# Performance work log

Measured on AMD Instinct MI355X. Metric: run time of the kernel, lower is better.

Reference implementation:

```python
import jax, jax.numpy as jnp
import numpy as np

H, DH = 8, 64            # heads, dim_head (module defaults)
B, N, DN, DE = 1, 512, 128, 64  # batch, nodes, node feat, edge feat
INNER = H * DH


def _w(key, fan_in, fan_out):
    return jax.random.normal(key, (fan_in, fan_out), jnp.float32) / np.sqrt(fan_in)


def setup_inputs() -> dict:
    key = jax.random.key(0)
    ks = jax.random.split(key, 8)
    return {
        "nodes": jax.random.normal(ks[0], (B, N, DN), jnp.float32),
        "edges": jax.random.normal(ks[1], (B, N, N, DE), jnp.float32),
        "mask": jnp.ones((B, N), dtype=bool),
        "Wq": _w(ks[2], DN, INNER), "bq": jnp.zeros((INNER,), jnp.float32),
        "Wk": _w(ks[3], DN, INNER), "bk": jnp.zeros((INNER,), jnp.float32),
        "Wv": _w(ks[4], DN, INNER), "bv": jnp.zeros((INNER,), jnp.float32),
        "We": _w(ks[5], DE, INNER), "be": jnp.zeros((INNER,), jnp.float32),
        "Wo": _w(ks[6], INNER, DN), "bo": jnp.zeros((DN,), jnp.float32),
    }


def _split_heads(x):
    # (b, ..., h*d) -> (b*h, ..., d), matching rearrange 'b ... (h d) -> (b h) ... d'
    b = x.shape[0]
    mid = x.shape[1:-1]
    x = x.reshape(b, *mid, H, DH)
    x = jnp.moveaxis(x, -2, 1)              # (b, h, ..., d)
    return x.reshape(b * H, *mid, DH)


def reference(nodes, edges, mask, Wq, bq, Wk, bk, Wv, bv, We, be, Wo, bo):
    scale = DH ** (-0.5)
    q = _split_heads(nodes @ Wq + bq)        # (bh, n, d)
    k = _split_heads(nodes @ Wk + bk)        # (bh, n, d)
    v = _split_heads(nodes @ Wv + bv)        # (bh, n, d)
    e = _split_heads(edges @ We + be)        # (bh, n, n, d) -- ek == ev == e_kv
    k = k[:, None, :, :] + e                 # (bh, i, j, d) per-ij keys
    v = v[:, None, :, :] + e                 # (bh, i, j, d) per-ij values
    sim = jnp.einsum('bid,bijd->bij', q, k) * scale
    m = mask[:, :, None] & mask[:, None, :]  # (b, i, j)
    m = jnp.repeat(m, H, axis=0)             # (bh, i, j)
    sim = jnp.where(m, sim, -jnp.finfo(sim.dtype).max)
    attn = jax.nn.softmax(sim, axis=-1)
    out = jnp.einsum('bij,bijd->bid', attn, v)           # (bh, n, d)
    out = out.reshape(B, H, N, DH).transpose(0, 2, 1, 3).reshape(B, N, INNER)
    return out @ Wo + bo                                  # (b, n, d_node)
```

## Files before the change

kernel.cpp:

```cpp
#include <hip/hip_runtime.h>
#include <hip/hip_bf16.h>

#define NN 512
#define DNODE 128
#define DEDGE 64
#define NH 8
#define DHD 64
#define DIN 512
#define SCALE 0.125f

typedef unsigned short u16;
typedef unsigned int u32;
typedef short bf16x8 __attribute__((ext_vector_type(8)));
typedef float f32x4 __attribute__((ext_vector_type(4)));

__device__ __forceinline__ float bf2f(u16 b) {
    u32 u = ((u32)b) << 16;
    return __builtin_bit_cast(float, u);
}
__device__ __forceinline__ u16 f2bf(float f) {
    u32 u = __builtin_bit_cast(u32, f);
    return (u16)((u + 0x7fffu + ((u >> 16) & 1u)) >> 16);
}
__device__ __forceinline__ float bflo(u32 u) { return __builtin_bit_cast(float, u << 16); }
__device__ __forceinline__ float bfhi(u32 u) { return __builtin_bit_cast(float, u & 0xffff0000u); }

__global__ __launch_bounds__(256) void k_qkv(
    const float* __restrict__ nodes,
    const float* __restrict__ Wq, const float* __restrict__ bq,
    const float* __restrict__ Wk, const float* __restrict__ bk,
    const float* __restrict__ Wv, const float* __restrict__ bv,
    float* __restrict__ Qo, float* __restrict__ Ko, float* __restrict__ Vo)
{
    const int it = blockIdx.x, ct = blockIdx.y, which = blockIdx.z;
    const float* W    = which == 0 ? Wq : (which == 1 ? Wk : Wv);
    const float* bias = which == 0 ? bq : (which == 1 ? bk : bv);
    float* O          = which == 0 ? Qo : (which == 1 ? Ko : Vo);
    __shared__ float As[64][132];
    __shared__ float Bs[128][68];
    const int t = threadIdx.x;
    const int ibase = it * 64, cbase = ct * 64;
#pragma unroll
    for (int p = 0; p < 8; ++p) {
        int r = p * 8 + (t >> 5), c4 = (t & 31) * 4;
        *(float4*)&As[r][c4] = *(const float4*)(nodes + (ibase + r) * DNODE + c4);
    }
#pragma unroll
    for (int p = 0; p < 8; ++p) {
        int k = p * 16 + (t >> 4), c4 = (t & 15) * 4;
        *(float4*)&Bs[k][c4] = *(const float4*)(W + k * DIN + cbase + c4);
    }
    __syncthreads();
    const int tx = t & 15, ty = t >> 4;
    float acc[4][4] = {};
    for (int k = 0; k < DNODE; ++k) {
        float4 b4 = *(const float4*)&Bs[k][tx * 4];
#pragma unroll
        for (int e = 0; e < 4; ++e) {
            float a = As[ty * 4 + e][k];
            acc[e][0] += a * b4.x; acc[e][1] += a * b4.y;
            acc[e][2] += a * b4.z; acc[e][3] += a * b4.w;
        }
    }
    const int h = ct;
#pragma unroll
    for (int ii = 0; ii < 4; ++ii) {
        int i = ibase + ty * 4 + ii;
        float4 o;
        o.x = acc[ii][0] + bias[cbase + tx * 4 + 0];
        o.y = acc[ii][1] + bias[cbase + tx * 4 + 1];
        o.z = acc[ii][2] + bias[cbase + tx * 4 + 2];
        o.w = acc[ii][3] + bias[cbase + tx * 4 + 3];
        *(float4*)(O + ((size_t)h * NN + i) * DHD + tx * 4) = o;
    }
}

__global__ __launch_bounds__(256) void k_qe(
    const float* __restrict__ Q, const float* __restrict__ We, float* __restrict__ QE)
{
    const int it = blockIdx.x, h = blockIdx.y;
    __shared__ float Qs[64][68];
    __shared__ float WsT[64][68];
    const int t = threadIdx.x;
    const int ibase = it * 64;
#pragma unroll
    for (int p = 0; p < 4; ++p) {
        int r = p * 16 + (t >> 4), d4 = (t & 15) * 4;
        *(float4*)&Qs[r][d4] = *(const float4*)(Q + ((size_t)h * NN + ibase + r) * DHD + d4);
    }
#pragma unroll
    for (int p = 0; p < 4; ++p) {
        int c = p * 16 + (t >> 4), d4 = (t & 15) * 4;
        float4 v = *(const float4*)(We + c * DIN + h * DHD + d4);
        WsT[d4 + 0][c] = v.x; WsT[d4 + 1][c] = v.y;
        WsT[d4 + 2][c] = v.z; WsT[d4 + 3][c] = v.w;
    }
    __syncthreads();
    const int tx = t & 15, ty = t >> 4;
    float acc[4][4] = {};
    for (int d = 0; d < DHD; ++d) {
        float4 b4 = *(const float4*)&WsT[d][tx * 4];
#pragma unroll
        for (int e = 0; e < 4; ++e) {
            float a = Qs[ty * 4 + e][d];
            acc[e][0] += a * b4.x; acc[e][1] += a * b4.y;
            acc[e][2] += a * b4.z; acc[e][3] += a * b4.w;
        }
    }
#pragma unroll
    for (int ii = 0; ii < 4; ++ii) {
        int i = ibase + ty * 4 + ii;
        float4 o;
        o.x = SCALE * acc[ii][0]; o.y = SCALE * acc[ii][1];
        o.z = SCALE * acc[ii][2]; o.w = SCALE * acc[ii][3];
        *(float4*)(QE + ((size_t)h * NN + i) * DEDGE + tx * 4) = o;
    }
}

__global__ __launch_bounds__(256) void k_qk(
    const float* __restrict__ Q, const float* __restrict__ K, float* __restrict__ QK)
{
    const int jt = blockIdx.x, it = blockIdx.y, h = blockIdx.z;
    __shared__ float Qs[64][68];
    __shared__ float KsT[64][68];
    const int t = threadIdx.x;
    const int ibase = it * 64, jbase = jt * 64;
#pragma unroll
    for (int p = 0; p < 4; ++p) {
        int r = p * 16 + (t >> 4), d4 = (t & 15) * 4;
        *(float4*)&Qs[r][d4] = *(const float4*)(Q + ((size_t)h * NN + ibase + r) * DHD + d4);
    }
#pragma unroll
    for (int p = 0; p < 4; ++p) {
        int j = p * 16 + (t >> 4), d4 = (t & 15) * 4;
        float4 v = *(const float4*)(K + ((size_t)h * NN + jbase + j) * DHD + d4);
        KsT[d4 + 0][j] = v.x; KsT[d4 + 1][j] = v.y;
        KsT[d4 + 2][j] = v.z; KsT[d4 + 3][j] = v.w;
    }
    __syncthreads();
    const int tx = t & 15, ty = t >> 4;
    float acc[4][4] = {};
    for (int d = 0; d < DHD; ++d) {
        float4 b4 = *(const float4*)&KsT[d][tx * 4];
#pragma unroll
        for (int e = 0; e < 4; ++e) {
            float a = Qs[ty * 4 + e][d];
            acc[e][0] += a * b4.x; acc[e][1] += a * b4.y;
            acc[e][2] += a * b4.z; acc[e][3] += a * b4.w;
        }
    }
#pragma unroll
    for (int ii = 0; ii < 4; ++ii) {
        int i = ibase + ty * 4 + ii;
        float4 o;
        o.x = SCALE * acc[ii][0]; o.y = SCALE * acc[ii][1];
        o.z = SCALE * acc[ii][2]; o.w = SCALE * acc[ii][3];
        *(float4*)(QK + ((size_t)h * NN + i) * NN + jbase + tx * 4) = o;
    }
}

__global__ __launch_bounds__(512, 4) void k_fused(
    const float* __restrict__ edges, const float* __restrict__ QK,
    const float* __restrict__ QE, float* __restrict__ AE, u16* __restrict__ P)
{
    __shared__ u16 erow[NN * 64];
    __shared__ u16 PlT[NH * 520];
    __shared__ float ae_acc[NH * 65];
    __shared__ float wred0[16][9];
    __shared__ float wred1[16][9];
    const int i = blockIdx.x;
    const int t = threadIdx.x;
    const int lane = t & 63, w = t >> 6;
    const int jl = lane & 15, hq = lane >> 4;
    const int h0 = hq * 4;
    const int jw = w * 64;

    const float* E = edges + (size_t)i * NN * DEDGE;
    const int jst = t >> 3, c0 = (t & 7) * 8;
    float4 fa[8], fb[8];
#pragma unroll
    for (int p = 0; p < 8; ++p) {
        const float* s = E + (p * 64 + jst) * 64 + c0;
        fa[p] = *(const float4*)s;
        fb[p] = *(const float4*)(s + 4);
    }
    float qkv[16];
#pragma unroll
    for (int jt = 0; jt < 4; ++jt)
#pragma unroll
        for (int r = 0; r < 4; ++r)
            qkv[jt * 4 + r] = (hq < 2)
                ? QK[((size_t)(h0 + r) * NN + i) * NN + jw + jt * 16 + jl] : 0.f;
    float4 qa0 = {0,0,0,0}, qa1 = qa0, qa2 = qa0, qa3 = qa0;
    if (jl < 8) {
        const float* qe = QE + ((size_t)jl * NN + i) * DEDGE + hq * 8;
        qa0 = *(const float4*)(qe + 0);
        qa1 = *(const float4*)(qe + 4);
        qa2 = *(const float4*)(qe + 32);
        qa3 = *(const float4*)(qe + 36);
    }
    for (int z = t; z < NH * 65; z += 512) ae_acc[z] = 0.f;

    bf16x8 af0, af1;
    af0[0]=(short)f2bf(qa0.x); af0[1]=(short)f2bf(qa0.y); af0[2]=(short)f2bf(qa0.z); af0[3]=(short)f2bf(qa0.w);
    af0[4]=(short)f2bf(qa1.x); af0[5]=(short)f2bf(qa1.y); af0[6]=(short)f2bf(qa1.z); af0[7]=(short)f2bf(qa1.w);
    af1[0]=(short)f2bf(qa2.x); af1[1]=(short)f2bf(qa2.y); af1[2]=(short)f2bf(qa2.z); af1[3]=(short)f2bf(qa2.w);
    af1[4]=(short)f2bf(qa3.x); af1[5]=(short)f2bf(qa3.y); af1[6]=(short)f2bf(qa3.z); af1[7]=(short)f2bf(qa3.w);

#pragma unroll
    for (int p = 0; p < 8; ++p) {
        int j = p * 64 + jst;
        uint4 pk;
        pk.x = (u32)f2bf(fa[p].x) | ((u32)f2bf(fa[p].y) << 16);
        pk.y = (u32)f2bf(fa[p].z) | ((u32)f2bf(fa[p].w) << 16);
        pk.z = (u32)f2bf(fb[p].x) | ((u32)f2bf(fb[p].y) << 16);
        pk.w = (u32)f2bf(fb[p].z) | ((u32)f2bf(fb[p].w) << 16);
        int sb = (j * 128 + c0 * 2) ^ ((j & 7) << 4);
        *(uint4*)((char*)erow + sb) = pk;
    }
    __syncthreads();

    f32x4 acc[4] = {f32x4{0,0,0,0}, f32x4{0,0,0,0}, f32x4{0,0,0,0}, f32x4{0,0,0,0}};
    const char* eb = (const char*)erow;
#pragma unroll
    for (int jt = 0; jt < 4; ++jt) {
        int j = jw + jt * 16 + jl;
        int x = (j & 7) << 4;
        uint4 e0 = *(const uint4*)(eb + ((j * 128 + hq * 16) ^ x));
        uint4 e1 = *(const uint4*)(eb + ((j * 128 + 64 + hq * 16) ^ x));
        f32x4 a = acc[jt];
        a = __builtin_amdgcn_mfma_f32_16x16x32_bf16(af0, __builtin_bit_cast(bf16x8, e0), a, 0, 0, 0);
        a = __builtin_amdgcn_mfma_f32_16x16x32_bf16(af1, __builtin_bit_cast(bf16x8, e1), a, 0, 0, 0);
        acc[jt] = a;
    }
#pragma unroll
    for (int jt = 0; jt < 4; ++jt)
#pragma unroll
        for (int r = 0; r < 4; ++r) acc[jt][r] += qkv[jt * 4 + r];

    float lred[4];
#pragma unroll
    for (int r = 0; r < 4; ++r) {
        float m0 = fmaxf(fmaxf(acc[0][r], acc[1][r]), fmaxf(acc[2][r], acc[3][r]));
        m0 = fmaxf(m0, __shfl_xor(m0, 1));
        m0 = fmaxf(m0, __shfl_xor(m0, 2));
        m0 = fmaxf(m0, __shfl_xor(m0, 4));
        m0 = fmaxf(m0, __shfl_xor(m0, 8));
        lred[r] = m0;
    }
    if (jl == 0 && hq < 2) {
#pragma unroll
        for (int r = 0; r < 4; ++r) wred0[h0 + r][w] = lred[r];
    }
    __syncthreads();
    float mm[4];
#pragma unroll
    for (int r = 0; r < 4; ++r) {
        float m = wred0[h0 + r][0];
#pragma unroll
        for (int ww = 1; ww < 8; ++ww) m = fmaxf(m, wred0[h0 + r][ww]);
        mm[r] = m;
    }
#pragma unroll
    for (int r = 0; r < 4; ++r) {
        float ls = 0.f;
#pragma unroll
        for (int jt = 0; jt < 4; ++jt) {
            float e = __expf(acc[jt][r] - mm[r]);
            acc[jt][r] = e; ls += e;
        }
        ls += __shfl_xor(ls, 1);
        ls += __shfl_xor(ls, 2);
        ls += __shfl_xor(ls, 4);
        ls += __shfl_xor(ls, 8);
        lred[r] = ls;
    }
    if (jl == 0 && hq < 2) {
#pragma unroll
        for (int r = 0; r < 4; ++r) wred1[h0 + r][w] = lred[r];
    }
    __syncthreads();
    if (hq < 2) {
#pragma unroll
        for (int r = 0; r < 4; ++r) {
            float s = wred1[h0 + r][0];
#pragma unroll
            for (int ww = 1; ww < 8; ++ww) s += wred1[h0 + r][ww];
            float inv = 1.f / s;
            int h = h0 + r;
#pragma unroll
            for (int jt = 0; jt < 4; ++jt) {
                int j = jw + jt * 16 + jl;
                u16 pb = f2bf(acc[jt][r] * inv);
                PlT[h * 520 + j] = pb;
                P[((size_t)h * NN + i) * NN + j] = pb;
            }
        }
    }
    __syncthreads();

    const int cp = lane & 31, jh = lane >> 5;
    const int jbase = w * 64 + jh * 32;
    float ae0[8] = {}, ae1[8] = {};
#pragma unroll
    for (int jb = 0; jb < 4; ++jb) {
        int j0 = jbase + jb * 8;
        float elo[8], ehi[8];
#pragma unroll
        for (int k = 0; k < 8; ++k) {
            int j = j0 + k;
            u32 ew = *(const u32*)((const char*)erow +
                      ((j * 128 + cp * 4) ^ ((j & 7) << 4)));
            elo[k] = bflo(ew); ehi[k] = bfhi(ew);
        }
#pragma unroll
        for (int h = 0; h < 8; ++h) {
            uint4 pv = *(const uint4*)&PlT[h * 520 + j0];
            float p0 = bflo(pv.x), p1 = bfhi(pv.x), p2 = bflo(pv.y), p3 = bfhi(pv.y);
            float p4 = bflo(pv.z), p5 = bfhi(pv.z), p6 = bflo(pv.w), p7 = bfhi(pv.w);
            ae0[h] += p0 * elo[0] + p1 * elo[1] + p2 * elo[2] + p3 * elo[3]
                    + p4 * elo[4] + p5 * elo[5] + p6 * elo[6] + p7 * elo[7];
            ae1[h] += p0 * ehi[0] + p1 * ehi[1] + p2 * ehi[2] + p3 * ehi[3]
                    + p4 * ehi[4] + p5 * ehi[5] + p6 * ehi[6] + p7 * ehi[7];
        }
    }
#pragma unroll
    for (int h = 0; h < 8; ++h) {
        ae0[h] += __shfl_xor(ae0[h], 32, 64);
        ae1[h] += __shfl_xor(ae1[h], 32, 64);
    }
    if (lane < 32) {
#pragma unroll
        for (int h = 0; h < 8; ++h) {
            atomicAdd(&ae_acc[h * 65 + 2 * cp],     ae0[h]);
            atomicAdd(&ae_acc[h * 65 + 2 * cp + 1], ae1[h]);
        }
    }
    __syncthreads();
    AE[(((size_t)(t >> 6)) * NN + i) * DEDGE + (t & 63)] = ae_acc[(t >> 6) * 65 + (t & 63)];
}

__global__ __launch_bounds__(256) void k_pv(
    const u16* __restrict__ P, const float* __restrict__ V, float* __restrict__ OUTV)
{
    const int ks = blockIdx.x, it = blockIdx.y, h = blockIdx.z;
    __shared__ u16 Ps[64][136];
    __shared__ float Vs[128][68];
    const int t = threadIdx.x;
    const int ibase = it * 64, kbase = ks * 128;
#pragma unroll
    for (int p = 0; p < 4; ++p) {
        int r = p * 16 + (t >> 4), j8 = (t & 15) * 8;
        *(uint4*)&Ps[r][j8] = *(const uint4*)(P + ((size_t)h * NN + ibase + r) * NN + kbase + j8);
    }
#pragma unroll
    for (int p = 0; p < 8; ++p) {
        int j = p * 16 + (t >> 4), d4 = (t & 15) * 4;
        *(float4*)&Vs[j][d4] = *(const float4*)(V + ((size_t)h * NN + kbase + j) * DHD + d4);
    }
    __syncthreads();
    const int tx = t & 15, ty = t >> 4;
    float acc[4][4] = {};
    for (int k = 0; k < 128; ++k) {
        float4 b4 = *(const float4*)&Vs[k][tx * 4];
#pragma unroll
        for (int e = 0; e < 4; ++e) {
            float a = bf2f(Ps[ty * 4 + e][k]);
            acc[e][0] += a * b4.x; acc[e][1] += a * b4.y;
            acc[e][2] += a * b4.z; acc[e][3] += a * b4.w;
        }
    }
#pragma unroll
    for (int ii = 0; ii < 4; ++ii)
#pragma unroll
        for (int jj = 0; jj < 4; ++jj)
            unsafeAtomicAdd(&OUTV[((size_t)h * NN + ibase + ty * 4 + ii) * DHD + tx * 4 + jj],
                            acc[ii][jj]);
}

__global__ __launch_bounds__(256) void k_inner(
    const float* __restrict__ AE, const float* __restrict__ We, const float* __restrict__ be,
    const float* __restrict__ OUTV, float* __restrict__ INNER)
{
    const int it = blockIdx.x, h = blockIdx.y;
    __shared__ float AEs[64][68];
    __shared__ float Ws[64][68];
    const int t = threadIdx.x;
    const int ibase = it * 64;
#pragma unroll
    for (int p = 0; p < 4; ++p) {
        int r = p * 16 + (t >> 4), c4 = (t & 15) * 4;
        *(float4*)&AEs[r][c4] = *(const float4*)(AE + ((size_t)h * NN + ibase + r) * DEDGE + c4);
    }
#pragma unroll
    for (int p = 0; p < 4; ++p) {
        int c = p * 16 + (t >> 4), d4 = (t & 15) * 4;
        *(float4*)&Ws[c][d4] = *(const float4*)(We + c * DIN + h * DHD + d4);
    }
    __syncthreads();
    const int tx = t & 15, ty = t >> 4;
    float acc[4][4] = {};
    for (int c = 0; c < DEDGE; ++c) {
        float4 b4 = *(const float4*)&Ws[c][tx * 4];
#pragma unroll
        for (int e = 0; e < 4; ++e) {
            float a = AEs[ty * 4 + e][c];
            acc[e][0] += a * b4.x; acc[e][1] += a * b4.y;
            acc[e][2] += a * b4.z; acc[e][3] += a * b4.w;
        }
    }
#pragma unroll
    for (int ii = 0; ii < 4; ++ii) {
        int i = ibase + ty * 4 + ii;
        float4 ov = *(const float4*)(OUTV + ((size_t)h * NN + i) * DHD + tx * 4);
        float4 o;
        o.x = acc[ii][0] + ov.x + be[h * DHD + tx * 4 + 0];
        o.y = acc[ii][1] + ov.y + be[h * DHD + tx * 4 + 1];
        o.z = acc[ii][2] + ov.z + be[h * DHD + tx * 4 + 2];
        o.w = acc[ii][3] + ov.w + be[h * DHD + tx * 4 + 3];
        *(float4*)(INNER + (size_t)i * DIN + h * DHD + tx * 4) = o;
    }
}

__global__ __launch_bounds__(256) void k_out(
    const float* __restrict__ INNER, const float* __restrict__ Wo, const float* __restrict__ bo,
    float* __restrict__ out)
{
    const int ks = blockIdx.x, it = blockIdx.y;
    __shared__ float Is[64][68];
    __shared__ float Wos[64][136];
    const int t = threadIdx.x;
    const int ibase = it * 64, kbase = ks * 64;
#pragma unroll
    for (int p = 0; p < 4; ++p) {
        int r = p * 16 + (t >> 4), c4 = (t & 15) * 4;
        *(float4*)&Is[r][c4] = *(const float4*)(INNER + (size_t)(ibase + r) * DIN + kbase + c4);
    }
#pragma unroll
    for (int p = 0; p < 8; ++p) {
        int k = p * 8 + (t >> 5), n4 = (t & 31) * 4;
        *(float4*)&Wos[k][n4] = *(const float4*)(Wo + (size_t)(kbase + k) * DNODE + n4);
    }
    __syncthreads();
    const int tx = t & 15, ty = t >> 4;
    float acc[4][8] = {};
    for (int k = 0; k < 64; ++k) {
        float4 b0 = *(const float4*)&Wos[k][tx * 8];
        float4 b1 = *(const float4*)&Wos[k][tx * 8 + 4];
#pragma unroll
        for (int e = 0; e < 4; ++e) {
            float a = Is[ty * 4 + e][k];
            acc[e][0] += a * b0.x; acc[e][1] += a * b0.y;
            acc[e][2] += a * b0.z; acc[e][3] += a * b0.w;
            acc[e][4] += a * b1.x; acc[e][5] += a * b1.y;
            acc[e][6] += a * b1.z; acc[e][7] += a * b1.w;
        }
    }
#pragma unroll
    for (int ii = 0; ii < 4; ++ii)
#pragma unroll
        for (int nn = 0; nn < 8; ++nn) {
            float v = acc[ii][nn] + (ks == 0 ? bo[tx * 8 + nn] : 0.f);
            unsafeAtomicAdd(&out[(size_t)(ibase + ty * 4 + ii) * DNODE + tx * 8 + nn], v);
        }
}

extern "C" void kernel_launch(void* const* d_in, const int* in_sizes, int n_in,
                              void* d_out, int out_size, void* d_ws, size_t ws_size,
                              hipStream_t stream) {
    (void)in_sizes; (void)n_in; (void)out_size; (void)ws_size;
    const float* nodes = (const float*)d_in[0];
    const float* edges = (const float*)d_in[1];
    const float* Wq = (const float*)d_in[3];  const float* bq = (const float*)d_in[4];
    const float* Wk = (const float*)d_in[5];  const float* bk = (const float*)d_in[6];
    const float* Wv = (const float*)d_in[7];  const float* bv = (const float*)d_in[8];
    const float* We = (const float*)d_in[9];  const float* be = (const float*)d_in[10];
    const float* Wo = (const float*)d_in[11]; const float* bo = (const float*)d_in[12];
    float* out = (float*)d_out;

    float* ws    = (float*)d_ws;
    float* Qb    = ws;
    float* Kb    = Qb    + NH * NN * DHD;
    float* Vb    = Kb    + NH * NN * DHD;
    float* QEb   = Vb    + NH * NN * DHD;
    float* AEb   = QEb   + NH * NN * DHD;
    float* OUTVb = AEb   + NH * NN * DHD;
    float* INb   = OUTVb + NH * NN * DHD;
    float* QKb   = INb   + (size_t)NN * DIN;
    u16*   Pb    = (u16*)(QKb + (size_t)NH * NN * NN);

    hipMemsetAsync(OUTVb, 0, (size_t)NH * NN * DHD * sizeof(float), stream);
    hipMemsetAsync(out, 0, (size_t)NN * DNODE * sizeof(float), stream);

    k_qkv<<<dim3(8, 8, 3), 256, 0, stream>>>(nodes, Wq, bq, Wk, bk, Wv, bv, Qb, Kb, Vb);
    k_qe<<<dim3(8, 8), 256, 0, stream>>>(Qb, We, QEb);
    k_qk<<<dim3(8, 8, 8), 256, 0, stream>>>(Qb, Kb, QKb);
    k_fused<<<dim3(512), 512, 0, stream>>>(edges, QKb, QEb, AEb, Pb);
    k_pv<<<dim3(4, 8, 8), 256, 0, stream>>>(Pb, Vb, OUTVb);
    k_inner<<<dim3(8, 8), 256, 0, stream>>>(AEb, We, be, OUTVb, INb);
    k_out<<<dim3(8, 8), 256, 0, stream>>>(INb, Wo, bo, out);
}
```

Measured before the change: 214.2 us.

## Use MFMA for attention-weighted edge sum and make edge staging wave-local

```diff
diff --git a/kernel.cpp b/kernel.cpp
--- a/kernel.cpp
+++ b/kernel.cpp
@@ -13,6 +13,7 @@
 typedef unsigned int u32;
 typedef short bf16x8 __attribute__((ext_vector_type(8)));
 typedef float f32x4 __attribute__((ext_vector_type(4)));
+typedef float fx4 __attribute__((ext_vector_type(4)));
 
 __device__ __forceinline__ float bf2f(u16 b) {
     u32 u = ((u32)b) << 16;
@@ -176,14 +177,30 @@
     const int jw = w * 64;
 
     const float* E = edges + (size_t)i * NN * DEDGE;
-    const int jst = t >> 3, c0 = (t & 7) * 8;
-    float4 fa[8], fb[8];
-#pragma unroll
-    for (int p = 0; p < 8; ++p) {
-        const float* s = E + (p * 64 + jst) * 64 + c0;
-        fa[p] = *(const float4*)s;
-        fb[p] = *(const float4*)(s + 4);
-    }
+    const int jst = jw + (lane >> 3);
+    const int c0 = (lane & 7) * 8;
+    fx4 fa[8], fb[8];
+#pragma unroll
+    for (int p = 0; p < 8; ++p) {
+        const float* s = E + (size_t)(jst + p * 8) * 64 + c0;
+        fa[p] = *(const fx4*)s;
+        fb[p] = *(const fx4*)(s + 4);
+    }
+#pragma unroll
+    for (int p = 0; p < 8; ++p) asm volatile("" : "+v"(fa[p]), "+v"(fb[p]));
+#pragma unroll
+    for (int p = 0; p < 8; ++p) {
+        int j = jst + p * 8;
+        uint4 pk;
+        pk.x = (u32)f2bf(fa[p][0]) | ((u32)f2bf(fa[p][1]) << 16);
+        pk.y = (u32)f2bf(fa[p][2]) | ((u32)f2bf(fa[p][3]) << 16);
+        pk.z = (u32)f2bf(fb[p][0]) | ((u32)f2bf(fb[p][1]) << 16);
+        pk.w = (u32)f2bf(fb[p][2]) | ((u32)f2bf(fb[p][3]) << 16);
+        int sb = (j * 128 + c0 * 2) ^ ((j & 7) << 4);
+        *(uint4*)((char*)erow + sb) = pk;
+    }
+    for (int z = t; z < NH * 65; z += 512) ae_acc[z] = 0.f;
+
     float qkv[16];
 #pragma unroll
     for (int jt = 0; jt < 4; ++jt)
@@ -191,34 +208,19 @@
         for (int r = 0; r < 4; ++r)
             qkv[jt * 4 + r] = (hq < 2)
                 ? QK[((size_t)(h0 + r) * NN + i) * NN + jw + jt * 16 + jl] : 0.f;
-    float4 qa0 = {0,0,0,0}, qa1 = qa0, qa2 = qa0, qa3 = qa0;
+    fx4 qa0 = {0,0,0,0}, qa1 = qa0, qa2 = qa0, qa3 = qa0;
     if (jl < 8) {
         const float* qe = QE + ((size_t)jl * NN + i) * DEDGE + hq * 8;
-        qa0 = *(const float4*)(qe + 0);
-        qa1 = *(const float4*)(qe + 4);
-        qa2 = *(const float4*)(qe + 32);
-        qa3 = *(const float4*)(qe + 36);
-    }
-    for (int z = t; z < NH * 65; z += 512) ae_acc[z] = 0.f;
-
+        qa0 = *(const fx4*)(qe + 0);
+        qa1 = *(const fx4*)(qe + 4);
+        qa2 = *(const fx4*)(qe + 32);
+        qa3 = *(const fx4*)(qe + 36);
+    }
     bf16x8 af0, af1;
-    af0[0]=(short)f2bf(qa0.x); af0[1]=(short)f2bf(qa0.y); af0[2]=(short)f2bf(qa0.z); af0[3]=(short)f2bf(qa0.w);
-    af0[4]=(short)f2bf(qa1.x); af0[5]=(short)f2bf(qa1.y); af0[6]=(short)f2bf(qa1.z); af0[7]=(short)f2bf(qa1.w);
-    af1[0]=(short)f2bf(qa2.x); af1[1]=(short)f2bf(qa2.y); af1[2]=(short)f2bf(qa2.z); af1[3]=(short)f2bf(qa2.w);
-    af1[4]=(short)f2bf(qa3.x); af1[5]=(short)f2bf(qa3.y); af1[6]=(short)f2bf(qa3.z); af1[7]=(short)f2bf(qa3.w);
-
-#pragma unroll
-    for (int p = 0; p < 8; ++p) {
-        int j = p * 64 + jst;
-        uint4 pk;
-        pk.x = (u32)f2bf(fa[p].x) | ((u32)f2bf(fa[p].y) << 16);
-        pk.y = (u32)f2bf(fa[p].z) | ((u32)f2bf(fa[p].w) << 16);
-        pk.z = (u32)f2bf(fb[p].x) | ((u32)f2bf(fb[p].y) << 16);
-        pk.w = (u32)f2bf(fb[p].z) | ((u32)f2bf(fb[p].w) << 16);
-        int sb = (j * 128 + c0 * 2) ^ ((j & 7) << 4);
-        *(uint4*)((char*)erow + sb) = pk;
-    }
-    __syncthreads();
+    af0[0]=(short)f2bf(qa0[0]); af0[1]=(short)f2bf(qa0[1]); af0[2]=(short)f2bf(qa0[2]); af0[3]=(short)f2bf(qa0[3]);
+    af0[4]=(short)f2bf(qa1[0]); af0[5]=(short)f2bf(qa1[1]); af0[6]=(short)f2bf(qa1[2]); af0[7]=(short)f2bf(qa1[3]);
+    af1[0]=(short)f2bf(qa2[0]); af1[1]=(short)f2bf(qa2[1]); af1[2]=(short)f2bf(qa2[2]); af1[3]=(short)f2bf(qa2[3]);
+    af1[4]=(short)f2bf(qa3[0]); af1[5]=(short)f2bf(qa3[1]); af1[6]=(short)f2bf(qa3[2]); af1[7]=(short)f2bf(qa3[3]);
 
     f32x4 acc[4] = {f32x4{0,0,0,0}, f32x4{0,0,0,0}, f32x4{0,0,0,0}, f32x4{0,0,0,0}};
     const char* eb = (const char*)erow;
@@ -297,44 +299,31 @@
             }
         }
     }
-    __syncthreads();
-
-    const int cp = lane & 31, jh = lane >> 5;
-    const int jbase = w * 64 + jh * 32;
-    float ae0[8] = {}, ae1[8] = {};
-#pragma unroll
-    for (int jb = 0; jb < 4; ++jb) {
-        int j0 = jbase + jb * 8;
-        float elo[8], ehi[8];
-#pragma unroll
-        for (int k = 0; k < 8; ++k) {
-            int j = j0 + k;
-            u32 ew = *(const u32*)((const char*)erow +
-                      ((j * 128 + cp * 4) ^ ((j & 7) << 4)));
-            elo[k] = bflo(ew); ehi[k] = bfhi(ew);
-        }
-#pragma unroll
-        for (int h = 0; h < 8; ++h) {
-            uint4 pv = *(const uint4*)&PlT[h * 520 + j0];
-            float p0 = bflo(pv.x), p1 = bfhi(pv.x), p2 = bflo(pv.y), p3 = bfhi(pv.y);
-            float p4 = bflo(pv.z), p5 = bfhi(pv.z), p6 = bflo(pv.w), p7 = bfhi(pv.w);
-            ae0[h] += p0 * elo[0] + p1 * elo[1] + p2 * elo[2] + p3 * elo[3]
-                    + p4 * elo[4] + p5 * elo[5] + p6 * elo[6] + p7 * elo[7];
-            ae1[h] += p0 * ehi[0] + p1 * ehi[1] + p2 * ehi[2] + p3 * ehi[3]
-                    + p4 * ehi[4] + p5 * ehi[5] + p6 * ehi[6] + p7 * ehi[7];
-        }
-    }
-#pragma unroll
-    for (int h = 0; h < 8; ++h) {
-        ae0[h] += __shfl_xor(ae0[h], 32, 64);
-        ae1[h] += __shfl_xor(ae1[h], 32, 64);
-    }
-    if (lane < 32) {
-#pragma unroll
-        for (int h = 0; h < 8; ++h) {
-            atomicAdd(&ae_acc[h * 65 + 2 * cp],     ae0[h]);
-            atomicAdd(&ae_acc[h * 65 + 2 * cp + 1], ae1[h]);
-        }
+
+    f32x4 ae4[4] = {f32x4{0,0,0,0}, f32x4{0,0,0,0}, f32x4{0,0,0,0}, f32x4{0,0,0,0}};
+#pragma unroll
+    for (int kt2 = 0; kt2 < 2; ++kt2) {
+        bf16x8 pa = {0,0,0,0,0,0,0,0};
+        if (jl < 8)
+            pa = *(const bf16x8*)&PlT[jl * 520 + jw + kt2 * 32 + hq * 8];
+        const int jb = jw + kt2 * 32 + hq * 8;
+#pragma unroll
+        for (int ct = 0; ct < 4; ++ct) {
+            const int cc = ct * 16 + jl;
+            bf16x8 bfr;
+#pragma unroll
+            for (int idx = 0; idx < 8; ++idx) {
+                bfr[idx] = (short)*(const u16*)(eb + (((jb + idx) * 128 + cc * 2) ^ (idx << 4)));
+            }
+            ae4[ct] = __builtin_amdgcn_mfma_f32_16x16x32_bf16(pa, bfr, ae4[ct], 0, 0, 0);
+        }
+    }
+    if (hq < 2) {
+#pragma unroll
+        for (int ct = 0; ct < 4; ++ct)
+#pragma unroll
+            for (int r = 0; r < 4; ++r)
+                atomicAdd(&ae_acc[(h0 + r) * 65 + ct * 16 + jl], ae4[ct][r]);
     }
     __syncthreads();
     AE[(((size_t)(t >> 6)) * NN + i) * DEDGE + (t & 63)] = ae_acc[(t >> 6) * 65 + (t & 63)];
```

Result: no change. 211.5 us (-1.2%).
